# Optimization experiments

Measured on AMD Instinct MI355X. Metric: run time of the kernel, lower is better.

Reference implementation:

```python
import jax, jax.numpy as jnp
import numpy as np

D_MODEL = 768
NHEAD = 12
HEAD_DIM = D_MODEL // NHEAD


def setup_inputs() -> dict:
    key = jax.random.key(0)
    ks = jax.random.split(key, 9)
    B, S = 1, 4096
    scale = 1.0 / np.sqrt(D_MODEL)
    x = jax.random.normal(ks[0], (B, S, D_MODEL), dtype=jnp.float32)
    # Linear params: weight [out,in] torch convention, bias [out]
    wq = jax.random.normal(ks[1], (D_MODEL, D_MODEL), dtype=jnp.float32) * scale
    bq = jnp.zeros((D_MODEL,), dtype=jnp.float32)
    wk = jax.random.normal(ks[2], (D_MODEL, D_MODEL), dtype=jnp.float32) * scale
    bk = jnp.zeros((D_MODEL,), dtype=jnp.float32)
    wv = jax.random.normal(ks[3], (D_MODEL, D_MODEL), dtype=jnp.float32) * scale
    bv = jnp.zeros((D_MODEL,), dtype=jnp.float32)
    wo = jax.random.normal(ks[4], (D_MODEL, D_MODEL), dtype=jnp.float32) * scale
    bo = jnp.zeros((D_MODEL,), dtype=jnp.float32)
    return {"x": x, "wq": wq, "bq": bq, "wk": wk, "bk": bk,
            "wv": wv, "bv": bv, "wo": wo, "bo": bo}


def reference(x, wq, bq, wk, bk, wv, bv, wo, bo):
    B, S, D = x.shape
    H, Hd = NHEAD, HEAD_DIM
    # projections (torch Linear: x @ W^T + b)
    q = (x @ wq.T + bq).reshape(B, S, H, Hd).transpose(0, 2, 1, 3)  # [B,H,S,Hd]
    k = (x @ wk.T + bk).reshape(B, S, H, Hd).transpose(0, 2, 1, 3)
    v = (x @ wv.T + bv).reshape(B, S, H, Hd).transpose(0, 2, 1, 3)
    scores = jnp.einsum('bhsd,bhtd->bhst', q, k) / jnp.sqrt(jnp.float32(Hd))  # [B,H,S,S]
    probs = jax.nn.softmax(scores, axis=-1)
    attn = jnp.einsum('bhst,bhtd->bhsd', probs, v)  # [B,H,S,Hd]
    attn = attn.transpose(0, 2, 1, 3).reshape(B, S, D)
    return attn @ wo.T + bo
```

## Files before the change

kernel.cpp:

```cpp
#include <hip/hip_runtime.h>
#include <hip/hip_bf16.h>

typedef __attribute__((ext_vector_type(8))) __bf16 bf16x8;
typedef __attribute__((ext_vector_type(4))) __bf16 bf16x4;
typedef __attribute__((ext_vector_type(4))) float f32x4;
typedef __attribute__((ext_vector_type(16))) float f32x16;
typedef __attribute__((ext_vector_type(2))) unsigned u32x2;

#define D_MODEL 768
#define SEQ     4096
#define NH      12
#define HD      64

#define QSCALE (0.125f * 1.44269504088896f)

__device__ __forceinline__ void gload_lds16(const void* g, void* l) {
    __builtin_amdgcn_global_load_lds(
        (const __attribute__((address_space(1))) void*)g,
        (__attribute__((address_space(3))) void*)l, 16, 0, 0);
}

__device__ __forceinline__ u32x2 plswap(unsigned a, unsigned b) {
    return __builtin_amdgcn_permlane32_swap(a, b, false, false);
}

__global__ __launch_bounds__(256) void cvt_kernel(
    const float* __restrict__ x,  const float* __restrict__ wq,
    const float* __restrict__ wk, const float* __restrict__ wv,
    const float* __restrict__ wo,
    __bf16* __restrict__ xb,  __bf16* __restrict__ wqb,
    __bf16* __restrict__ wkb, __bf16* __restrict__ wvb,
    __bf16* __restrict__ wob)
{
    const int XV = SEQ * D_MODEL / 4;
    const int WV = D_MODEL * D_MODEL / 4;
    const int total = XV + 4 * WV;
    for (int i = blockIdx.x * blockDim.x + threadIdx.x; i < total;
         i += gridDim.x * blockDim.x) {
        const float* src; __bf16* dst; int j;
        if      (i < XV)          { src = x;  dst = xb;  j = i; }
        else if (i < XV + WV)     { src = wq; dst = wqb; j = i - XV; }
        else if (i < XV + 2*WV)   { src = wk; dst = wkb; j = i - XV - WV; }
        else if (i < XV + 3*WV)   { src = wv; dst = wvb; j = i - XV - 2*WV; }
        else                      { src = wo; dst = wob; j = i - XV - 3*WV; }
        float4 v = ((const float4*)src)[j];
        bf16x4 o;
        o[0] = (__bf16)v.x; o[1] = (__bf16)v.y;
        o[2] = (__bf16)v.z; o[3] = (__bf16)v.w;
        ((bf16x4*)dst)[j] = o;
    }
}

__device__ __forceinline__ void gemm128_core(
    const __bf16* __restrict__ A, const __bf16* __restrict__ B, int KD,
    f32x4 acc[4][4], __bf16 (*As)[128][64], __bf16 (*Bs)[128][64])
{
    const int t = threadIdx.x;
    const int lane = t & 63, wid = t >> 6;
    const int wm = (wid & 1) * 64, wn = (wid >> 1) * 64;
    const int lr = lane & 15, lc = lane >> 4;
    const int rl = lane >> 3;
    const int cs = (lane & 7) ^ rl;

    const __bf16* ag = A + (size_t)(wid * 32 + rl) * KD + cs * 8;
    const __bf16* bg = B + (size_t)(wid * 32 + rl) * KD + cs * 8;

#define GSTAGE(BUF, KT) do {                                                  \
        _Pragma("unroll")                                                     \
        for (int i = 0; i < 4; ++i) {                                         \
            gload_lds16(ag + (size_t)i * 8 * KD + (KT) * 64,                  \
                        &As[BUF][wid * 32 + i * 8][0]);                       \
            gload_lds16(bg + (size_t)i * 8 * KD + (KT) * 64,                  \
                        &Bs[BUF][wid * 32 + i * 8][0]);                       \
        }                                                                     \
    } while (0)

#define GCOMP(BUF) do {                                                       \
        _Pragma("unroll")                                                     \
        for (int kh = 0; kh < 2; ++kh) {                                      \
            bf16x8 af[4], bfr[4];                                             \
            _Pragma("unroll")                                                 \
            for (int mi = 0; mi < 4; ++mi)                                    \
                af[mi] = *(const bf16x8*)                                     \
                    &As[BUF][wm + mi*16 + lr][(((kh<<2)|lc) ^ (lr&7)) * 8];   \
            _Pragma("unroll")                                                 \
            for (int ni = 0; ni < 4; ++ni)                                    \
                bfr[ni] = *(const bf16x8*)                                    \
                    &Bs[BUF][wn + ni*16 + lr][(((kh<<2)|lc) ^ (lr&7)) * 8];   \
            __builtin_amdgcn_s_setprio(1);                                    \
            _Pragma("unroll")                                                 \
            for (int mi = 0; mi < 4; ++mi)                                    \
                _Pragma("unroll")                                             \
                for (int ni = 0; ni < 4; ++ni)                                \
                    acc[mi][ni] = __builtin_amdgcn_mfma_f32_16x16x32_bf16(    \
                        af[mi], bfr[ni], acc[mi][ni], 0, 0, 0);               \
            __builtin_amdgcn_s_setprio(0);                                    \
        }                                                                     \
    } while (0)

    GSTAGE(0, 0);
    const int NK = KD / 64;
    for (int kt = 0; kt < NK; kt += 2) {
        __builtin_amdgcn_s_barrier();
        GSTAGE(1, kt + 1);
        asm volatile("s_waitcnt vmcnt(8)" ::: "memory");
        __builtin_amdgcn_s_barrier();
        GCOMP(0);
        __builtin_amdgcn_s_barrier();
        if (kt + 2 < NK) {
            GSTAGE(0, kt + 2);
            asm volatile("s_waitcnt vmcnt(8)" ::: "memory");
        } else {
            asm volatile("s_waitcnt vmcnt(0)" ::: "memory");
        }
        __builtin_amdgcn_s_barrier();
        GCOMP(1);
    }
#undef GSTAGE
#undef GCOMP
}

__global__ __launch_bounds__(256) void qkv_gemm(
    const __bf16* __restrict__ xb,
    const __bf16* __restrict__ wqb, const __bf16* __restrict__ wkb,
    const __bf16* __restrict__ wvb,
    const float* __restrict__ bq, const float* __restrict__ bk,
    const float* __restrict__ bv,
    __bf16* __restrict__ Qo, __bf16* __restrict__ Ko,
    __bf16* __restrict__ Vto)
{
    __shared__ __bf16 As[2][128][64];
    __shared__ __bf16 Bs[2][128][64];
    const int b = blockIdx.x;
    const int swz = (b & 7) * 72 + (b >> 3);
    const int bm = swz & 31;
    const int yy = swz >> 5;
    const int seg = yy / 6, bn = yy % 6;
    const __bf16* B  = (seg == 0) ? wqb : (seg == 1) ? wkb : wvb;
    const float* bias = (seg == 0) ? bq : (seg == 1) ? bk : bv;

    f32x4 acc[4][4] = {};
    gemm128_core(xb + (size_t)bm * 128 * D_MODEL,
                 B  + (size_t)bn * 128 * D_MODEL, D_MODEL, acc, As, Bs);

    const int t = threadIdx.x, lane = t & 63, wid = t >> 6;
    const int wm = (wid & 1) * 64, wn = (wid >> 1) * 64;
    const int lr = lane & 15, lc = lane >> 4;
    const int m0 = bm * 128 + wm, n0 = bn * 128 + wn;

    if (seg < 2) {
        __bf16* O = (seg == 0) ? Qo : Ko;
        const float sc = (seg == 0) ? QSCALE : 1.0f;
        #pragma unroll
        for (int mi = 0; mi < 4; ++mi)
            #pragma unroll
            for (int ni = 0; ni < 4; ++ni) {
                int col = n0 + ni * 16 + lr;
                float bb = bias[col];
                #pragma unroll
                for (int r = 0; r < 4; ++r)
                    O[(size_t)(m0 + mi * 16 + lc * 4 + r) * D_MODEL + col] =
                        (__bf16)((acc[mi][ni][r] + bb) * sc);
            }
    } else {
        #pragma unroll
        for (int mi = 0; mi < 4; ++mi)
            #pragma unroll
            for (int ni = 0; ni < 4; ++ni) {
                int col = n0 + ni * 16 + lr;
                float bb = bias[col];
                bf16x4 pk;
                #pragma unroll
                for (int r = 0; r < 4; ++r)
                    pk[r] = (__bf16)(acc[mi][ni][r] + bb);
                *(bf16x4*)&Vto[(size_t)col * SEQ + m0 + mi * 16 + lc * 4] = pk;
            }
    }
}

__global__ __launch_bounds__(256) void attn_kernel(
    const __bf16* __restrict__ Q, const __bf16* __restrict__ K,
    const __bf16* __restrict__ Vt, __bf16* __restrict__ Attn)
{
    __shared__ __align__(16) char LDSc[49152];
    __bf16 (*Ks)[32][64] = (__bf16(*)[32][64])(LDSc);
    __bf16 (*Vs)[64][32] = (__bf16(*)[64][32])(LDSc + 24576);
    float* Mg = (float*)LDSc;
    float* Ml = (float*)(LDSc + 24576);

    const int bid = blockIdx.x;
    const int swz = (bid & 7) * 96 + (bid >> 3);
    const int h  = swz >> 6;
    const int q0 = (swz & 63) * 64;

    const int t = threadIdx.x, lane = t & 63, wid = t >> 6;
    const int qs = wid & 1, half = wid >> 1;
    const int ql = lane & 31, hi = lane >> 5;
    const int s7 = ql & 7;
    const int v2s = (ql >> 1) & 3;

    const int krl = lane >> 3, kcs = (lane & 7) ^ (lane >> 3);
    const int vrl = lane >> 2, vcs = (lane & 3) ^ ((lane >> 3) & 3);
    const __bf16* kg = K +
        (size_t)(half * 2048 + qs * 16 + krl) * D_MODEL + h * HD + kcs * 8;
    const __bf16* vg = Vt +
        (size_t)(h * HD + qs * 32 + vrl) * SEQ + half * 2048 + vcs * 8;

    const __bf16* qrow = Q + (size_t)(q0 + qs * 32 + ql) * D_MODEL + h * HD;
    bf16x8 qf[4];
    #pragma unroll
    for (int k4 = 0; k4 < 4; ++k4)
        qf[k4] = *(const bf16x8*)&qrow[k4 * 16 + hi * 8];

    f32x16 acc0 = {}, acc1 = {};
    f32x16 lacc = {};

    #define STAGE(BUF, TT) do {                                               \
        const __bf16* kgt = kg + (size_t)(TT) * 32 * D_MODEL;                 \
        const __bf16* vgt = vg + (TT) * 32;                                   \
        gload_lds16(kgt,                    &Ks[half*3 + (BUF)][qs*16][0]);   \
        gload_lds16(kgt + 8 * D_MODEL,      &Ks[half*3 + (BUF)][qs*16+8][0]); \
        gload_lds16(vgt,                    &Vs[half*3 + (BUF)][qs*32][0]);   \
        gload_lds16(vgt + (size_t)16 * SEQ, &Vs[half*3 + (BUF)][qs*32+16][0]);\
    } while (0)

    STAGE(0, 0);

    const int NT = 2048 / 32;

#define ATILE(CUR, NXT, PT, DOPF) do {                                        \
    if (DOPF) {                                                               \
        STAGE(NXT, PT);                                                       \
        asm volatile("s_waitcnt vmcnt(4)" ::: "memory");                      \
    } else {                                                                  \
        asm volatile("s_waitcnt vmcnt(0)" ::: "memory");                      \
    }                                                                         \
    __builtin_amdgcn_s_barrier();                                             \
    f32x16 st = {};                                                           \
    __builtin_amdgcn_s_setprio(1);                                            \
    _Pragma("unroll")                                                         \
    for (int k4 = 0; k4 < 4; ++k4) {                                          \
        bf16x8 kf = *(const bf16x8*)                                          \
            &Ks[half*3 + (CUR)][ql][((k4*2 + hi) ^ s7) * 8];                  \
        st = __builtin_amdgcn_mfma_f32_32x32x16_bf16(kf, qf[k4], st, 0,0,0);  \
    }                                                                         \
    __builtin_amdgcn_s_setprio(0);                                            \
                 \
    _Pragma("unroll")                                                         \
    for (int r = 0; r < 16; ++r) st[r] = exp2f(st[r]);                        \
    lacc += st;                                                               \
                                               \
    unsigned wA[4], wB[4];                                                    \
    _Pragma("unroll")                                                         \
    for (int g = 0; g < 4; ++g) {                                             \
        union { __bf16 h2[2]; unsigned u; } pa, pb;                           \
        pa.h2[0] = (__bf16)st[4*g + 0]; pa.h2[1] = (__bf16)st[4*g + 1];       \
        pb.h2[0] = (__bf16)st[4*g + 2]; pb.h2[1] = (__bf16)st[4*g + 3];       \
        wA[g] = pa.u; wB[g] = pb.u;                                           \
    }                                                                         \
    __builtin_amdgcn_s_setprio(1);                                            \
    _Pragma("unroll")                                                         \
    for (int kb = 0; kb < 2; ++kb) {                                          \
        u32x2 sA = plswap(wA[2*kb], wA[2*kb + 1]);                            \
        u32x2 sB = plswap(wB[2*kb], wB[2*kb + 1]);                            \
        union { unsigned u[4]; bf16x8 v; } fb;                                \
        fb.u[0] = sA[0]; fb.u[1] = sB[0]; fb.u[2] = sA[1]; fb.u[3] = sB[1];   \
        bf16x8 vf0 = *(const bf16x8*)                                         \
            &Vs[half*3 + (CUR)][ql][((kb*2 + hi) ^ v2s) * 8];                 \
        bf16x8 vf1 = *(const bf16x8*)                                         \
            &Vs[half*3 + (CUR)][32 + ql][((kb*2 + hi) ^ v2s) * 8];            \
        acc0 = __builtin_amdgcn_mfma_f32_32x32x16_bf16(vf0, fb.v, acc0,0,0,0);\
        acc1 = __builtin_amdgcn_mfma_f32_32x32x16_bf16(vf1, fb.v, acc1,0,0,0);\
    }                                                                         \
    __builtin_amdgcn_s_setprio(0);                                            \
} while (0)

    for (int kk = 0; kk < 63; kk += 3) {
        ATILE(0, 1, kk + 1, 1);
        ATILE(1, 2, kk + 2, 1);
        ATILE(2, 0, kk + 3, (kk + 3 < NT));
    }
    ATILE(0, 1, 0, 0);
#undef ATILE
#undef STAGE

    float l_r;
    {
        float t8[8];
        #pragma unroll
        for (int i = 0; i < 8; ++i) t8[i] = lacc[i] + lacc[i + 8];
        #pragma unroll
        for (int i = 0; i < 4; ++i) t8[i] += t8[i + 4];
        l_r = (t8[0] + t8[1]) + (t8[2] + t8[3]);
        u32x2 rp = plswap(__float_as_uint(l_r), __float_as_uint(l_r));
        l_r = __uint_as_float(rp[0]) + __uint_as_float(rp[1]);
    }

    __syncthreads();
    if (half == 1) {
        float* mybuf = Mg + qs * 2048 + lane * 32;
        #pragma unroll
        for (int j = 0; j < 4; ++j) {
            f32x4 v; v[0]=acc0[4*j]; v[1]=acc0[4*j+1]; v[2]=acc0[4*j+2]; v[3]=acc0[4*j+3];
            *(f32x4*)&mybuf[(j ^ s7) * 4] = v;
        }
        #pragma unroll
        for (int j = 0; j < 4; ++j) {
            f32x4 v; v[0]=acc1[4*j]; v[1]=acc1[4*j+1]; v[2]=acc1[4*j+2]; v[3]=acc1[4*j+3];
            *(f32x4*)&mybuf[((4 + j) ^ s7) * 4] = v;
        }
        Ml[qs * 64 + lane] = l_r;
    }
    __syncthreads();
    if (half == 0) {
        float l1 = Ml[qs * 64 + lane];
        float li = 1.0f / (l_r + l1);
        const float* obuf = Mg + qs * 2048 + lane * 32;

        __bf16* orow = Attn + (size_t)(q0 + qs * 32 + ql) * D_MODEL
                       + h * HD + hi * 4;
        #pragma unroll
        for (int g = 0; g < 4; ++g) {
            f32x4 a1 = *(const f32x4*)&obuf[(g ^ s7) * 4];
            union { __bf16 h4[4]; uint2 v2; } w;
            #pragma unroll
            for (int i = 0; i < 4; ++i)
                w.h4[i] = (__bf16)((acc0[4*g+i] + a1[i]) * li);
            *(uint2*)&orow[g * 8] = w.v2;

            f32x4 b1 = *(const f32x4*)&obuf[((4 + g) ^ s7) * 4];
            #pragma unroll
            for (int i = 0; i < 4; ++i)
                w.h4[i] = (__bf16)((acc1[4*g+i] + b1[i]) * li);
            *(uint2*)&orow[32 + g * 8] = w.v2;
        }
    }
}

__global__ __launch_bounds__(256) void out_gemm(
    const __bf16* __restrict__ Ab, const __bf16* __restrict__ wob,
    const float* __restrict__ bo, float* __restrict__ out)
{
    __shared__ __bf16 As[2][128][64];
    __shared__ __bf16 Bs[2][128][64];
    const int b = blockIdx.x;
    const int swz = (b & 7) * 24 + (b >> 3);
    const int bm = swz & 31, bn = swz >> 5;
    f32x4 acc[4][4] = {};
    gemm128_core(Ab  + (size_t)bm * 128 * D_MODEL,
                 wob + (size_t)bn * 128 * D_MODEL, D_MODEL, acc, As, Bs);

    const int t = threadIdx.x, lane = t & 63, wid = t >> 6;
    const int wm = (wid & 1) * 64, wn = (wid >> 1) * 64;
    const int lr = lane & 15, lc = lane >> 4;
    const int m0 = bm * 128 + wm, n0 = bn * 128 + wn;
    #pragma unroll
    for (int mi = 0; mi < 4; ++mi)
        #pragma unroll
        for (int ni = 0; ni < 4; ++ni) {
            int col = n0 + ni * 16 + lr;
            float bb = bo[col];
            #pragma unroll
            for (int r = 0; r < 4; ++r)
                out[(size_t)(m0 + mi * 16 + lc * 4 + r) * D_MODEL + col] =
                    acc[mi][ni][r] + bb;
        }
}

extern "C" void kernel_launch(void* const* d_in, const int* in_sizes, int n_in,
                              void* d_out, int out_size, void* d_ws, size_t ws_size,
                              hipStream_t stream) {
    const float* x  = (const float*)d_in[0];
    const float* wq = (const float*)d_in[1];
    const float* bq = (const float*)d_in[2];
    const float* wk = (const float*)d_in[3];
    const float* bk = (const float*)d_in[4];
    const float* wv = (const float*)d_in[5];
    const float* bv = (const float*)d_in[6];
    const float* wo = (const float*)d_in[7];
    const float* bo = (const float*)d_in[8];

    char* ws = (char*)d_ws;
    const size_t XB_SZ = (size_t)SEQ * D_MODEL * 2;
    const size_t W_SZ  = (size_t)D_MODEL * D_MODEL * 2;
    __bf16* xb  = (__bf16*)(ws);
    __bf16* wqb = (__bf16*)(ws + XB_SZ);
    __bf16* wkb = (__bf16*)(ws + XB_SZ + W_SZ);
    __bf16* wvb = (__bf16*)(ws + XB_SZ + 2 * W_SZ);
    __bf16* wob = (__bf16*)(ws + XB_SZ + 3 * W_SZ);
    __bf16* Qb  = (__bf16*)(ws + XB_SZ + 4 * W_SZ);
    __bf16* Kb  = (__bf16*)(ws + 2 * XB_SZ + 4 * W_SZ);
    __bf16* Vtb = (__bf16*)(ws + 3 * XB_SZ + 4 * W_SZ);
    __bf16* Ab  = (__bf16*)(ws + 4 * XB_SZ + 4 * W_SZ);

    cvt_kernel<<<1024, 256, 0, stream>>>(x, wq, wk, wv, wo,
                                         xb, wqb, wkb, wvb, wob);
    qkv_gemm<<<576, 256, 0, stream>>>(xb, wqb, wkb, wvb,
                                      bq, bk, bv, Qb, Kb, Vtb);
    attn_kernel<<<768, 256, 0, stream>>>(Qb, Kb, Vtb, Ab);
    out_gemm<<<192, 256, 0, stream>>>(Ab, wob, bo, (float*)d_out);
}
```

Measured before the change: 151.0 us.

## Fuse fp32-to-bf16 conversion of output weight into output GEMM

Removes the wo conversion from the separate cvt kernel. out_gemm now reads fp32 wo directly, converts it to bf16 in registers, and stores it to LDS, using register-prefetch double buffering instead of the async global-to-LDS path in gemm128_core. This saves one weight write and read pass through memory. In exchange, each of the 192 blocks converts its slice of wo again, and the GEMM mainloop loses the direct LDS loads and double-buffered LDS.

```diff
diff --git a/kernel.cpp b/kernel.cpp
--- a/kernel.cpp
+++ b/kernel.cpp
@@ -24,25 +24,31 @@
     return __builtin_amdgcn_permlane32_swap(a, b, false, false);
 }
 
+__device__ __forceinline__ bf16x8 cvt8(const float4& a, const float4& b) {
+    union { __bf16 h8[8]; bf16x8 v; } p;
+    p.h8[0] = (__bf16)a.x; p.h8[1] = (__bf16)a.y;
+    p.h8[2] = (__bf16)a.z; p.h8[3] = (__bf16)a.w;
+    p.h8[4] = (__bf16)b.x; p.h8[5] = (__bf16)b.y;
+    p.h8[6] = (__bf16)b.z; p.h8[7] = (__bf16)b.w;
+    return p.v;
+}
+
 __global__ __launch_bounds__(256) void cvt_kernel(
     const float* __restrict__ x,  const float* __restrict__ wq,
     const float* __restrict__ wk, const float* __restrict__ wv,
-    const float* __restrict__ wo,
     __bf16* __restrict__ xb,  __bf16* __restrict__ wqb,
-    __bf16* __restrict__ wkb, __bf16* __restrict__ wvb,
-    __bf16* __restrict__ wob)
+    __bf16* __restrict__ wkb, __bf16* __restrict__ wvb)
 {
     const int XV = SEQ * D_MODEL / 4;
     const int WV = D_MODEL * D_MODEL / 4;
-    const int total = XV + 4 * WV;
+    const int total = XV + 3 * WV;
     for (int i = blockIdx.x * blockDim.x + threadIdx.x; i < total;
          i += gridDim.x * blockDim.x) {
         const float* src; __bf16* dst; int j;
         if      (i < XV)          { src = x;  dst = xb;  j = i; }
         else if (i < XV + WV)     { src = wq; dst = wqb; j = i - XV; }
         else if (i < XV + 2*WV)   { src = wk; dst = wkb; j = i - XV - WV; }
-        else if (i < XV + 3*WV)   { src = wv; dst = wvb; j = i - XV - 2*WV; }
-        else                      { src = wo; dst = wob; j = i - XV - 3*WV; }
+        else                      { src = wv; dst = wvb; j = i - XV - 2*WV; }
         float4 v = ((const float4*)src)[j];
         bf16x4 o;
         o[0] = (__bf16)v.x; o[1] = (__bf16)v.y;
@@ -338,21 +344,74 @@
 }
 
 __global__ __launch_bounds__(256) void out_gemm(
-    const __bf16* __restrict__ Ab, const __bf16* __restrict__ wob,
+    const __bf16* __restrict__ Ab, const float* __restrict__ wo,
     const float* __restrict__ bo, float* __restrict__ out)
 {
-    __shared__ __bf16 As[2][128][64];
-    __shared__ __bf16 Bs[2][128][64];
+    __shared__ __bf16 As[128][64];
+    __shared__ __bf16 Bs[128][64];
     const int b = blockIdx.x;
     const int swz = (b & 7) * 24 + (b >> 3);
     const int bm = swz & 31, bn = swz >> 5;
-    f32x4 acc[4][4] = {};
-    gemm128_core(Ab  + (size_t)bm * 128 * D_MODEL,
-                 wob + (size_t)bn * 128 * D_MODEL, D_MODEL, acc, As, Bs);
 
     const int t = threadIdx.x, lane = t & 63, wid = t >> 6;
     const int wm = (wid & 1) * 64, wn = (wid >> 1) * 64;
     const int lr = lane & 15, lc = lane >> 4;
+    const int r = t >> 1;
+    const int hb = (t & 1) * 4;
+
+    const __bf16* ax = Ab + (size_t)(bm * 128 + r) * D_MODEL + hb * 8;
+    const float*  bx = wo + (size_t)(bn * 128 + r) * D_MODEL + hb * 8;
+
+    f32x4 acc[4][4] = {};
+
+    bf16x8 av[4];
+    float4 bv8[8];
+    #pragma unroll
+    for (int j = 0; j < 4; ++j) av[j] = *(const bf16x8*)(ax + j * 8);
+    #pragma unroll
+    for (int j = 0; j < 8; ++j) bv8[j] = *(const float4*)(bx + j * 4);
+
+    const int NK = D_MODEL / 64;
+    for (int kt = 0; kt < NK; ++kt) {
+        __syncthreads();
+        #pragma unroll
+        for (int i = 0; i < 4; ++i) {
+            *(bf16x8*)&As[r][((hb + i) ^ (r & 7)) * 8] = av[i];
+            *(bf16x8*)&Bs[r][((hb + i) ^ (r & 7)) * 8] =
+                cvt8(bv8[2 * i], bv8[2 * i + 1]);
+        }
+        if (kt + 1 < NK) {
+            #pragma unroll
+            for (int j = 0; j < 4; ++j)
+                av[j] = *(const bf16x8*)(ax + (kt + 1) * 64 + j * 8);
+            #pragma unroll
+            for (int j = 0; j < 8; ++j)
+                bv8[j] = *(const float4*)(bx + (kt + 1) * 64 + j * 4);
+        }
+        __syncthreads();
+
+        #pragma unroll
+        for (int kh = 0; kh < 2; ++kh) {
+            bf16x8 af[4], bfr[4];
+            #pragma unroll
+            for (int mi = 0; mi < 4; ++mi)
+                af[mi] = *(const bf16x8*)
+                    &As[wm + mi * 16 + lr][(((kh << 2) | lc) ^ (lr & 7)) * 8];
+            #pragma unroll
+            for (int ni = 0; ni < 4; ++ni)
+                bfr[ni] = *(const bf16x8*)
+                    &Bs[wn + ni * 16 + lr][(((kh << 2) | lc) ^ (lr & 7)) * 8];
+            __builtin_amdgcn_s_setprio(1);
+            #pragma unroll
+            for (int mi = 0; mi < 4; ++mi)
+                #pragma unroll
+                for (int ni = 0; ni < 4; ++ni)
+                    acc[mi][ni] = __builtin_amdgcn_mfma_f32_16x16x32_bf16(
+                        af[mi], bfr[ni], acc[mi][ni], 0, 0, 0);
+            __builtin_amdgcn_s_setprio(0);
+        }
+    }
+
     const int m0 = bm * 128 + wm, n0 = bn * 128 + wn;
     #pragma unroll
     for (int mi = 0; mi < 4; ++mi)
@@ -361,9 +420,9 @@
             int col = n0 + ni * 16 + lr;
             float bb = bo[col];
             #pragma unroll
-            for (int r = 0; r < 4; ++r)
-                out[(size_t)(m0 + mi * 16 + lc * 4 + r) * D_MODEL + col] =
-                    acc[mi][ni][r] + bb;
+            for (int rr = 0; rr < 4; ++rr)
+                out[(size_t)(m0 + mi * 16 + lc * 4 + rr) * D_MODEL + col] =
+                    acc[mi][ni][rr] + bb;
         }
 }
 
@@ -387,16 +446,15 @@
     __bf16* wqb = (__bf16*)(ws + XB_SZ);
     __bf16* wkb = (__bf16*)(ws + XB_SZ + W_SZ);
     __bf16* wvb = (__bf16*)(ws + XB_SZ + 2 * W_SZ);
-    __bf16* wob = (__bf16*)(ws + XB_SZ + 3 * W_SZ);
-    __bf16* Qb  = (__bf16*)(ws + XB_SZ + 4 * W_SZ);
-    __bf16* Kb  = (__bf16*)(ws + 2 * XB_SZ + 4 * W_SZ);
-    __bf16* Vtb = (__bf16*)(ws + 3 * XB_SZ + 4 * W_SZ);
-    __bf16* Ab  = (__bf16*)(ws + 4 * XB_SZ + 4 * W_SZ);
-
-    cvt_kernel<<<1024, 256, 0, stream>>>(x, wq, wk, wv, wo,
-                                         xb, wqb, wkb, wvb, wob);
+    __bf16* Qb  = (__bf16*)(ws + XB_SZ + 3 * W_SZ);
+    __bf16* Kb  = (__bf16*)(ws + 2 * XB_SZ + 3 * W_SZ);
+    __bf16* Vtb = (__bf16*)(ws + 3 * XB_SZ + 3 * W_SZ);
+    __bf16* Ab  = (__bf16*)(ws + 4 * XB_SZ + 3 * W_SZ);
+
+    cvt_kernel<<<1024, 256, 0, stream>>>(x, wq, wk, wv,
+                                         xb, wqb, wkb, wvb);
     qkv_gemm<<<576, 256, 0, stream>>>(xb, wqb, wkb, wvb,
                                       bq, bk, bv, Qb, Kb, Vtb);
     attn_kernel<<<768, 256, 0, stream>>>(Qb, Kb, Vtb, Ab);
-    out_gemm<<<192, 256, 0, stream>>>(Ab, wob, bo, (float*)d_out);
-}
+    out_gemm<<<192, 256, 0, stream>>>(Ab, wo, bo, (float*)d_out);
+}
```

New measurement: 157.5 us. 4.3% more time.
